# Performance work log

Hardware: AMD Instinct MI355X
Metric: run time of the kernel (lower is better)

## Reference

```python
import jax, jax.numpy as jnp
import numpy as np


def setup_inputs() -> dict:
    key = jax.random.key(0)
    k = jax.random.split(key, 7)
    B, IN, OUT = 128, 1024, 1024
    return {
        "x": jax.random.normal(k[0], (B, IN), dtype=jnp.float32),
        "eps": jax.random.normal(k[1], (B, IN, OUT), dtype=jnp.float32),
        "eps_bias": jax.random.normal(k[2], (B, OUT), dtype=jnp.float32),
        "mu": jax.random.normal(k[3], (IN, OUT), dtype=jnp.float32),
        "ro": jax.random.normal(k[4], (IN, OUT), dtype=jnp.float32),
        "mu_bias": jax.random.normal(k[5], (1, OUT), dtype=jnp.float32),
        "ro_bias": jax.random.normal(k[6], (1, OUT), dtype=jnp.float32),
    }


def reference(x, eps, eps_bias, mu, ro, mu_bias, ro_bias):
    # softplus: log(1 + exp(ro)) as written in the original module
    sigma = jnp.log1p(jnp.exp(ro))            # [in, out]
    sigma_bias = jnp.log1p(jnp.exp(ro_bias))  # [1, out]
    weights = eps * sigma + mu                # [B, in, out] per-sample weights
    bias = eps_bias * sigma_bias + mu_bias    # [B, out]
    # (x.unsqueeze(1) @ weights).squeeze() -> per-sample matvec
    return jnp.einsum("bi,bio->bo", x, weights) + bias
```

## Files before the change

kernel.cpp:

```cpp
#include <hip/hip_runtime.h>
#include <math.h>

#define BB 128
#define IN 1024
#define OUTD 1024
#define ISPLIT 16
#define ICHUNK (IN / ISPLIT)

typedef float f4v __attribute__((ext_vector_type(4)));

__device__ __forceinline__ float softplus(float r) {
    return fmaxf(r, 0.0f) + log1pf(expf(-fabsf(r)));
}

__global__ __launch_bounds__(256) void prep_sm(const float* __restrict__ ro,
                                               const float* __restrict__ mu,
                                               float* __restrict__ sm) {
    int idx = blockIdx.x * 256 + threadIdx.x;
    float4 r = ((const float4*)ro)[idx];
    float4 m = ((const float4*)mu)[idx];
    float4 s;
    s.x = softplus(r.x);
    s.y = softplus(r.y);
    s.z = softplus(r.z);
    s.w = softplus(r.w);
    ((float4*)sm)[idx * 2] = s;
    ((float4*)sm)[idx * 2 + 1] = m;
}

__global__ __launch_bounds__(256, 2) void bayes_main(
    const float* __restrict__ x, const float* __restrict__ eps,
    const float* __restrict__ sm, float* __restrict__ partial) {
    __shared__ float xs[16][ICHUNK];
    const int tid = threadIdx.x;

    const int bid = blockIdx.x;
    const int xcd = bid & 7;
    const int t = bid >> 3;
    const int s_local = t & 7;
    const int bblk = t >> 3;
    const int slice = s_local * 8 + xcd;
    const int oblk = slice & 3;
    const int iblk = slice >> 2;
    const int b0 = bblk * 16;
    const int o0 = oblk * 256;
    const int i0 = iblk * ICHUNK;

    for (int tt = tid; tt < 16 * ICHUNK; tt += 256) {
        int bb = tt / ICHUNK, ii = tt % ICHUNK;
        xs[bb][ii] = x[(size_t)(b0 + bb) * IN + i0 + ii];
    }
    __syncthreads();

    const int oq = tid & 63;
    const int bsub = tid >> 6;
    const int o = o0 + oq * 4;

    const float4* smp = (const float4*)(sm + ((size_t)i0 * OUTD + o) * 2);
    const f4v* e0p =
        (const f4v*)(eps + ((size_t)(b0 + bsub) * IN + i0) * OUTD + o);
    const f4v* e1p =
        (const f4v*)(eps + ((size_t)(b0 + bsub + 4) * IN + i0) * OUTD + o);
    const f4v* e2p =
        (const f4v*)(eps + ((size_t)(b0 + bsub + 8) * IN + i0) * OUTD + o);
    const f4v* e3p =
        (const f4v*)(eps + ((size_t)(b0 + bsub + 12) * IN + i0) * OUTD + o);

    float4 acc0 = {0.f, 0.f, 0.f, 0.f};
    float4 acc1 = {0.f, 0.f, 0.f, 0.f};
    float4 acc2 = {0.f, 0.f, 0.f, 0.f};
    float4 acc3 = {0.f, 0.f, 0.f, 0.f};

#pragma unroll 4
    for (int ii = 0; ii < ICHUNK; ++ii) {
        float4 s = smp[(size_t)ii * (OUTD / 2)];
        float4 m = smp[(size_t)ii * (OUTD / 2) + 1];
        f4v e0 = __builtin_nontemporal_load(e0p + (size_t)ii * (OUTD / 4));
        f4v e1 = __builtin_nontemporal_load(e1p + (size_t)ii * (OUTD / 4));
        f4v e2 = __builtin_nontemporal_load(e2p + (size_t)ii * (OUTD / 4));
        f4v e3 = __builtin_nontemporal_load(e3p + (size_t)ii * (OUTD / 4));
        float x0 = xs[bsub][ii];
        float x1 = xs[bsub + 4][ii];
        float x2 = xs[bsub + 8][ii];
        float x3 = xs[bsub + 12][ii];
        acc0.x = fmaf(x0, fmaf(e0.x, s.x, m.x), acc0.x);
        acc0.y = fmaf(x0, fmaf(e0.y, s.y, m.y), acc0.y);
        acc0.z = fmaf(x0, fmaf(e0.z, s.z, m.z), acc0.z);
        acc0.w = fmaf(x0, fmaf(e0.w, s.w, m.w), acc0.w);
        acc1.x = fmaf(x1, fmaf(e1.x, s.x, m.x), acc1.x);
        acc1.y = fmaf(x1, fmaf(e1.y, s.y, m.y), acc1.y);
        acc1.z = fmaf(x1, fmaf(e1.z, s.z, m.z), acc1.z);
        acc1.w = fmaf(x1, fmaf(e1.w, s.w, m.w), acc1.w);
        acc2.x = fmaf(x2, fmaf(e2.x, s.x, m.x), acc2.x);
        acc2.y = fmaf(x2, fmaf(e2.y, s.y, m.y), acc2.y);
        acc2.z = fmaf(x2, fmaf(e2.z, s.z, m.z), acc2.z);
        acc2.w = fmaf(x2, fmaf(e2.w, s.w, m.w), acc2.w);
        acc3.x = fmaf(x3, fmaf(e3.x, s.x, m.x), acc3.x);
        acc3.y = fmaf(x3, fmaf(e3.y, s.y, m.y), acc3.y);
        acc3.z = fmaf(x3, fmaf(e3.z, s.z, m.z), acc3.z);
        acc3.w = fmaf(x3, fmaf(e3.w, s.w, m.w), acc3.w);
    }

    float* base = partial + ((size_t)iblk * BB) * OUTD + o;
    *(float4*)(base + (size_t)(b0 + bsub) * OUTD) = acc0;
    *(float4*)(base + (size_t)(b0 + bsub + 4) * OUTD) = acc1;
    *(float4*)(base + (size_t)(b0 + bsub + 8) * OUTD) = acc2;
    *(float4*)(base + (size_t)(b0 + bsub + 12) * OUTD) = acc3;
}

__global__ __launch_bounds__(256) void finalize(
    const float* __restrict__ partial, const float* __restrict__ eps_bias,
    const float* __restrict__ mu_bias, const float* __restrict__ ro_bias,
    float* __restrict__ out) {
    int idx = blockIdx.x * 256 + threadIdx.x;
    int p = idx * 4;
    int o = p & (OUTD - 1);

    float4 acc = {0.f, 0.f, 0.f, 0.f};
#pragma unroll
    for (int is = 0; is < ISPLIT; ++is) {
        float4 a = *(const float4*)(partial + (size_t)is * BB * OUTD + p);
        acc.x += a.x;
        acc.y += a.y;
        acc.z += a.z;
        acc.w += a.w;
    }
    float4 eb = *(const float4*)(eps_bias + p);
    float4 rb = *(const float4*)(ro_bias + o);
    float4 mb = *(const float4*)(mu_bias + o);

    float4 r;
    r.x = acc.x + eb.x * softplus(rb.x) + mb.x;
    r.y = acc.y + eb.y * softplus(rb.y) + mb.y;
    r.z = acc.z + eb.z * softplus(rb.z) + mb.z;
    r.w = acc.w + eb.w * softplus(rb.w) + mb.w;
    ((float4*)out)[idx] = r;
}

extern "C" void kernel_launch(void* const* d_in, const int* in_sizes, int n_in,
                              void* d_out, int out_size, void* d_ws, size_t ws_size,
                              hipStream_t stream) {
    const float* x = (const float*)d_in[0];
    const float* eps = (const float*)d_in[1];
    const float* eps_bias = (const float*)d_in[2];
    const float* mu = (const float*)d_in[3];
    const float* ro = (const float*)d_in[4];
    const float* mu_bias = (const float*)d_in[5];
    const float* ro_bias = (const float*)d_in[6];
    float* out = (float*)d_out;

    float* sm = (float*)d_ws;
    float* partial = sm + (size_t)2 * IN * OUTD;

    prep_sm<<<(IN * OUTD / 4) / 256, 256, 0, stream>>>(ro, mu, sm);

    bayes_main<<<512, 256, 0, stream>>>(x, eps, sm, partial);

    finalize<<<(BB * OUTD / 4) / 256, 256, 0, stream>>>(partial, eps_bias, mu_bias,
                                                        ro_bias, out);
}
```

Before: 104.3 us.

## Retile main kernel to full output row per block with four batches

Each block now covers all 1024 outputs for four consecutive batch rows and one 64-wide input chunk, replacing the old 256-output by 16-batch tile. The same four batches are shared by the whole block, so the x values in LDS become broadcast reads and the shared array shrinks. The block-to-XCD mapping changes so each XCD handles fixed input chunks. The cost is that the sigma and mu reads are reused across only four batches per block instead of sixteen, which raises traffic for those reads through the cache.

```diff
diff --git a/kernel.cpp b/kernel.cpp
--- a/kernel.cpp
+++ b/kernel.cpp
@@ -31,40 +31,30 @@
 __global__ __launch_bounds__(256, 2) void bayes_main(
     const float* __restrict__ x, const float* __restrict__ eps,
     const float* __restrict__ sm, float* __restrict__ partial) {
-    __shared__ float xs[16][ICHUNK];
+    __shared__ float xs[4][ICHUNK];
     const int tid = threadIdx.x;
 
     const int bid = blockIdx.x;
     const int xcd = bid & 7;
     const int t = bid >> 3;
-    const int s_local = t & 7;
-    const int bblk = t >> 3;
-    const int slice = s_local * 8 + xcd;
-    const int oblk = slice & 3;
-    const int iblk = slice >> 2;
-    const int b0 = bblk * 16;
-    const int o0 = oblk * 256;
+    const int iblk = xcd + 8 * (t & 1);
+    const int bblk = t >> 1;
+    const int b0 = bblk * 4;
     const int i0 = iblk * ICHUNK;
 
-    for (int tt = tid; tt < 16 * ICHUNK; tt += 256) {
-        int bb = tt / ICHUNK, ii = tt % ICHUNK;
+    {
+        int bb = tid >> 6, ii = tid & 63;
         xs[bb][ii] = x[(size_t)(b0 + bb) * IN + i0 + ii];
     }
     __syncthreads();
 
-    const int oq = tid & 63;
-    const int bsub = tid >> 6;
-    const int o = o0 + oq * 4;
+    const int o = tid * 4;
 
     const float4* smp = (const float4*)(sm + ((size_t)i0 * OUTD + o) * 2);
-    const f4v* e0p =
-        (const f4v*)(eps + ((size_t)(b0 + bsub) * IN + i0) * OUTD + o);
-    const f4v* e1p =
-        (const f4v*)(eps + ((size_t)(b0 + bsub + 4) * IN + i0) * OUTD + o);
-    const f4v* e2p =
-        (const f4v*)(eps + ((size_t)(b0 + bsub + 8) * IN + i0) * OUTD + o);
-    const f4v* e3p =
-        (const f4v*)(eps + ((size_t)(b0 + bsub + 12) * IN + i0) * OUTD + o);
+    const f4v* e0p = (const f4v*)(eps + ((size_t)(b0 + 0) * IN + i0) * OUTD + o);
+    const f4v* e1p = (const f4v*)(eps + ((size_t)(b0 + 1) * IN + i0) * OUTD + o);
+    const f4v* e2p = (const f4v*)(eps + ((size_t)(b0 + 2) * IN + i0) * OUTD + o);
+    const f4v* e3p = (const f4v*)(eps + ((size_t)(b0 + 3) * IN + i0) * OUTD + o);
 
     float4 acc0 = {0.f, 0.f, 0.f, 0.f};
     float4 acc1 = {0.f, 0.f, 0.f, 0.f};
@@ -79,10 +69,10 @@
         f4v e1 = __builtin_nontemporal_load(e1p + (size_t)ii * (OUTD / 4));
         f4v e2 = __builtin_nontemporal_load(e2p + (size_t)ii * (OUTD / 4));
         f4v e3 = __builtin_nontemporal_load(e3p + (size_t)ii * (OUTD / 4));
-        float x0 = xs[bsub][ii];
-        float x1 = xs[bsub + 4][ii];
-        float x2 = xs[bsub + 8][ii];
-        float x3 = xs[bsub + 12][ii];
+        float x0 = xs[0][ii];
+        float x1 = xs[1][ii];
+        float x2 = xs[2][ii];
+        float x3 = xs[3][ii];
         acc0.x = fmaf(x0, fmaf(e0.x, s.x, m.x), acc0.x);
         acc0.y = fmaf(x0, fmaf(e0.y, s.y, m.y), acc0.y);
         acc0.z = fmaf(x0, fmaf(e0.z, s.z, m.z), acc0.z);
@@ -102,10 +92,10 @@
     }
 
     float* base = partial + ((size_t)iblk * BB) * OUTD + o;
-    *(float4*)(base + (size_t)(b0 + bsub) * OUTD) = acc0;
-    *(float4*)(base + (size_t)(b0 + bsub + 4) * OUTD) = acc1;
-    *(float4*)(base + (size_t)(b0 + bsub + 8) * OUTD) = acc2;
-    *(float4*)(base + (size_t)(b0 + bsub + 12) * OUTD) = acc3;
+    *(float4*)(base + (size_t)(b0 + 0) * OUTD) = acc0;
+    *(float4*)(base + (size_t)(b0 + 1) * OUTD) = acc1;
+    *(float4*)(base + (size_t)(b0 + 2) * OUTD) = acc2;
+    *(float4*)(base + (size_t)(b0 + 3) * OUTD) = acc3;
 }
 
 __global__ __launch_bounds__(256) void finalize(
```

Result: slower. 110.8 us (+6.2%).
